# Kernel tuning notes

Hardware: AMD Instinct MI355X
Metric: run time of the kernel (lower is better)

The kernel has to match this reference:

```python
import jax, jax.numpy as jnp
import numpy as np

K = 3          # cfg.KNN_UP
CHUNK = 2048   # point chunk for brute-force KNN
BN_EPS = 1e-5


def knn_interp(vox_c, vox_f, pt_c):
    """Inverse-distance k-NN interpolation of voxel features onto points.
    vox_c: [Nv,3] voxel centers; vox_f: [Nv,C]; pt_c: [Np,3]. Returns [Np,C]."""
    Np = pt_c.shape[0]

    def chunk_fn(pc):  # pc: [CHUNK,3]
        d2 = jnp.sum((pc[:, None, :] - vox_c[None, :, :]) ** 2, axis=-1)  # [CHUNK,Nv]
        neg_d2, idx = jax.lax.top_k(-d2, K)                               # k nearest
        d = jnp.sqrt(jnp.maximum(-neg_d2, 0.0))
        w = 1.0 / (d + 1e-8)
        w = w / jnp.sum(w, axis=-1, keepdims=True)                        # [CHUNK,K]
        return jnp.sum(vox_f[idx] * w[..., None], axis=1)                 # [CHUNK,C]

    out = jax.lax.map(chunk_fn, pt_c.reshape(Np // CHUNK, CHUNK, 3))
    return out.reshape(Np, vox_f.shape[-1])


def bn1d(x, gamma, beta):
    # BatchNorm1d in training mode, applied per decomposed batch item (as in
    # the original per-sample list comprehension): stats over the point dim.
    mu = jnp.mean(x, axis=0, keepdims=True)
    var = jnp.var(x, axis=0, keepdims=True)
    return gamma * (x - mu) * jax.lax.rsqrt(var + BN_EPS) + beta


def level_forward(vox_c, vox_f, pt_c, gamma, beta):
    f = jax.vmap(knn_interp, in_axes=(0, 0, 0))(vox_c, vox_f, pt_c)  # [B,Np,C]
    return jax.vmap(lambda xf: bn1d(xf, gamma, beta))(f)


def setup_inputs() -> dict:
    key = jax.random.key(0)
    ks = jax.random.split(key, 16)
    B, Np = 2, 32768
    SCENE = 50.0  # spread coordinates over a ~50m scene
    nvs = [2048, 6144, 16384, 32768]
    chs = [256, 128, 96, 96]
    inp = {"pt_c": jax.random.uniform(ks[0], (B, Np, 3), jnp.float32) * SCENE}
    for i, (nv, c) in enumerate(zip(nvs, chs), start=1):
        inp[f"vox_c{i}"] = jax.random.uniform(ks[2 * i - 1], (B, nv, 3), jnp.float32) * SCENE
        inp[f"vox_f{i}"] = jax.random.normal(ks[2 * i], (B, nv, c), jnp.float32)
        inp[f"gamma{i}"] = jnp.ones((c,), jnp.float32)
        inp[f"beta{i}"] = jnp.zeros((c,), jnp.float32)
    return inp


def reference(pt_c, vox_c1, vox_f1, gamma1, beta1,
              vox_c2, vox_f2, gamma2, beta2,
              vox_c3, vox_f3, gamma3, beta3,
              vox_c4, vox_f4, gamma4, beta4):
    # voxel_to_point: per-level KNN upsampling of decoder voxel features to
    # the raw point cloud, followed by per-sample BatchNorm1d.
    f1 = level_forward(vox_c1, vox_f1, pt_c, gamma1, beta1)
    f2 = level_forward(vox_c2, vox_f2, pt_c, gamma2, beta2)
    f3 = level_forward(vox_c3, vox_f3, pt_c, gamma3, beta3)
    f4 = level_forward(vox_c4, vox_f4, pt_c, gamma4, beta4)
    return (f1, f2, f3, f4)
```

## Files before the change

kernel.cpp:

```cpp
#include <hip/hip_runtime.h>
#include <cfloat>
#include <climits>
#include <cstdint>

#define NPOINTS 32768
#define NBATCH  2
#define NLEV    4
#define NJOB    5
#define PG      16
#define PCELLS  (PG*PG*PG)
#define NPB     128
#define NBLK    (NPOINTS / NPB)

struct BinJob {
  const float* coords;
  int* cnt; int* start; int* cur;
  float4* sorted;
  int G, ncells, N;
  float invh;
};
struct BinParams { BinJob job[NJOB]; };

struct Level {
  const float4* sorted;
  const int*    start;
  int*          idxo;
  float*        wo;
  int G, ncells, Nv;
  float h, invh;
};
struct Params { Level lv[NLEV]; };

struct ApplyParams {
  const float* scale[NLEV];
  const float* shift[NLEV];
};

__device__ __forceinline__ int cell1d(float x, float invh, int G) {
  int c = (int)(x * invh);
  return min(max(c, 0), G - 1);
}

__global__ __launch_bounds__(256) void zero_kernel(int* __restrict__ p, int n)
{
  int i = blockIdx.x * 256 + threadIdx.x;
  if (i < n) p[i] = 0;
}

__global__ __launch_bounds__(256) void count_kernel(BinParams prm)
{
  const BinJob J = prm.job[blockIdx.z];
  int v = blockIdx.x * 256 + threadIdx.x;
  int b = blockIdx.y;
  if (v >= J.N) return;
  const float* p = J.coords + ((size_t)b * J.N + v) * 3;
  int cx = cell1d(p[0], J.invh, J.G), cy = cell1d(p[1], J.invh, J.G), cz = cell1d(p[2], J.invh, J.G);
  atomicAdd(&J.cnt[b * J.ncells + (cz * J.G + cy) * J.G + cx], 1);
}

__global__ __launch_bounds__(1024) void scan_kernel(BinParams prm)
{
  const BinJob J = prm.job[blockIdx.y];
  const int b = blockIdx.x, t = threadIdx.x;
  const int ncells = J.ncells;
  const int* c  = J.cnt + (size_t)b * ncells;
  int* st = J.start + (size_t)b * (ncells + 1);
  int* cu = J.cur + (size_t)b * ncells;
  __shared__ int part[1024];
  const int chunk = (ncells + 1023) / 1024;
  const int lo = t * chunk, hi = min(lo + chunk, ncells);
  int s = 0;
  for (int i = lo; i < hi; ++i) s += c[i];
  part[t] = s;
  __syncthreads();
  for (int off = 1; off < 1024; off <<= 1) {
    int v = (t >= off) ? part[t - off] : 0;
    __syncthreads();
    part[t] += v;
    __syncthreads();
  }
  int base = (t > 0) ? part[t - 1] : 0;
  for (int i = lo; i < hi; ++i) { st[i] = base; cu[i] = base; base += c[i]; }
  if (t == 1023) st[ncells] = part[1023];
}

__global__ __launch_bounds__(256) void scatter_kernel(BinParams prm)
{
  const BinJob J = prm.job[blockIdx.z];
  int v = blockIdx.x * 256 + threadIdx.x;
  int b = blockIdx.y;
  if (v >= J.N) return;
  const float* p = J.coords + ((size_t)b * J.N + v) * 3;
  float x = p[0], y = p[1], z = p[2];
  int cx = cell1d(x, J.invh, J.G), cy = cell1d(y, J.invh, J.G), cz = cell1d(z, J.invh, J.G);
  int pos = atomicAdd(&J.cur[b * J.ncells + (cz * J.G + cy) * J.G + cx], 1);
  J.sorted[(size_t)b * J.N + pos] = make_float4(x, y, z, __int_as_float(v));
}

__global__ __launch_bounds__(256) void phase1_kernel(
    const float4* __restrict__ psorted, Params prm,
    unsigned* __restrict__ taillist, int* __restrict__ tailcnt)
{
  const int l = blockIdx.y, b = blockIdx.z;
  const Level L = prm.lv[l];
  const int tid = threadIdx.x;
  const int q = tid & 3;
  const int sp = blockIdx.x * 64 + (tid >> 2);
  float4 pt = psorted[(size_t)b * NPOINTS + sp];
  const float px = pt.x, py = pt.y, pz = pt.z;
  const int p = __float_as_int(pt.w);
  const int G = L.G;
  const float h = L.h;

  const int cx = cell1d(px, L.invh, G);
  const int cy = cell1d(py, L.invh, G);
  const int cz = cell1d(pz, L.invh, G);
  const float fx = px - cx * h, fy = py - cy * h, fz = pz - cz * h;
  float m = fminf(fminf(fminf(fx, h - fx), fminf(fy, h - fy)), fminf(fz, h - fz));
  m = fmaxf(m, 0.f);

  const int* start     = L.start  + (size_t)b * (L.ncells + 1);
  const float4* sorted = L.sorted + (size_t)b * L.Nv;

  float b0 = FLT_MAX, b1 = FLT_MAX, b2 = FLT_MAX;
  int   i0 = INT_MAX, i1 = INT_MAX, i2 = INT_MAX;

  auto ins = [&](float d2, int vi) {
    if (d2 < b2 || (d2 == b2 && vi < i2)) {
      if (d2 < b1 || (d2 == b1 && vi < i1)) {
        b2 = b1; i2 = i1;
        if (d2 < b0 || (d2 == b0 && vi < i0)) { b1 = b0; i1 = i0; b0 = d2; i0 = vi; }
        else                                  { b1 = d2; i1 = vi; }
      } else { b2 = d2; i2 = vi; }
    }
  };
  auto cand = [&](int k) {
    float4 vv = sorted[k];
    int vi = __float_as_int(vv.w);
    float dx = px - vv.x, dy = py - vv.y, dz = pz - vv.z;
    float d2 = __fadd_rn(__fadd_rn(__fmul_rn(dx, dx), __fmul_rn(dy, dy)),
                         __fmul_rn(dz, dz));
    ins(d2, vi);
  };

  {
    const int x0 = max(cx - 1, 0), x1 = min(cx + 1, G - 1);
    int ks9[9], ke9[9];
    #pragma unroll
    for (int i = 0; i < 9; ++i) {
      const int dz = i / 3 - 1, dy = i % 3 - 1;
      const int iz = cz + dz, iy = cy + dy;
      const bool ok = (iz >= 0) && (iz < G) && (iy >= 0) && (iy < G);
      const int row = (iz * G + iy) * G;
      const int sa = ok ? (row + x0) : 0;
      const int sb = ok ? (row + x1 + 1) : 0;
      int a = start[sa], e = start[sb];
      if (!ok) { a = 0; e = 0; }
      ks9[i] = a; ke9[i] = e;
    }
    #pragma unroll
    for (int i = 0; i < 9; ++i)
      for (int k = ks9[i] + q; k < ke9[i]; k += 4) cand(k);
  }

  #pragma unroll
  for (int mask = 1; mask <= 2; mask <<= 1) {
    float c0 = __shfl_xor(b0, mask), c1 = __shfl_xor(b1, mask), c2 = __shfl_xor(b2, mask);
    int   j0 = __shfl_xor(i0, mask), j1 = __shfl_xor(i1, mask), j2 = __shfl_xor(i2, mask);
    ins(c0, j0); ins(c1, j1); ins(c2, j2);
  }

  float dmin = h + m;
  bool contained = (dmin * dmin * 0.99999f > b2);

  if (q == 0) {
    if (contained) {
      float w0 = 1.0f / (sqrtf(b0) + 1e-8f);
      float w1 = 1.0f / (sqrtf(b1) + 1e-8f);
      float w2 = 1.0f / (sqrtf(b2) + 1e-8f);
      float ws = (w0 + w1) + w2;
      size_t o = ((size_t)b * NPOINTS + p) * 3;
      L.idxo[o] = i0; L.idxo[o + 1] = i1; L.idxo[o + 2] = i2;
      L.wo[o] = w0 / ws; L.wo[o + 1] = w1 / ws; L.wo[o + 2] = w2 / ws;
    } else {
      int slot = atomicAdd(tailcnt, 1);
      taillist[slot] = (unsigned)sp | ((unsigned)l << 15) | ((unsigned)b << 17);
    }
  }
}

__global__ __launch_bounds__(256) void tail_kernel(
    const float4* __restrict__ psorted, Params prm,
    const unsigned* __restrict__ taillist, const int* __restrict__ tailcnt)
{
  const int tid = threadIdx.x;
  const int q = tid & 3;
  const int ent = blockIdx.x * 64 + (tid >> 2);
  const int n = *tailcnt;
  if (ent >= n) return;

  unsigned e = taillist[ent];
  const int sp = e & 0x7fff;
  const int l  = (e >> 15) & 3;
  const int b  = (e >> 17) & 1;
  const Level L = prm.lv[l];
  float4 pt = psorted[(size_t)b * NPOINTS + sp];
  const float px = pt.x, py = pt.y, pz = pt.z;
  const int p = __float_as_int(pt.w);
  const int G = L.G;
  const float h = L.h;

  const int cx = cell1d(px, L.invh, G);
  const int cy = cell1d(py, L.invh, G);
  const int cz = cell1d(pz, L.invh, G);
  const float fx = px - cx * h, fy = py - cy * h, fz = pz - cz * h;
  float m = fminf(fminf(fminf(fx, h - fx), fminf(fy, h - fy)), fminf(fz, h - fz));
  m = fmaxf(m, 0.f);

  const int* start     = L.start  + (size_t)b * (L.ncells + 1);
  const float4* sorted = L.sorted + (size_t)b * L.Nv;

  float b0 = FLT_MAX, b1 = FLT_MAX, b2 = FLT_MAX;
  int   i0 = INT_MAX, i1 = INT_MAX, i2 = INT_MAX;

  auto ins = [&](float d2, int vi) {
    if (d2 < b2 || (d2 == b2 && vi < i2)) {
      if (d2 < b1 || (d2 == b1 && vi < i1)) {
        b2 = b1; i2 = i1;
        if (d2 < b0 || (d2 == b0 && vi < i0)) { b1 = b0; i1 = i0; b0 = d2; i0 = vi; }
        else                                  { b1 = d2; i1 = vi; }
      } else { b2 = d2; i2 = vi; }
    }
  };
  auto cand = [&](int k) {
    float4 vv = sorted[k];
    int vi = __float_as_int(vv.w);
    float dx = px - vv.x, dy = py - vv.y, dz = pz - vv.z;
    float d2 = __fadd_rn(__fadd_rn(__fmul_rn(dx, dx), __fmul_rn(dy, dy)),
                         __fmul_rn(dz, dz));
    ins(d2, vi);
  };
  auto scan_range = [&](int ks, int ke) {
    for (int k = ks + q; k < ke; k += 4) cand(k);
  };

  const int rmax = max(max(cx, G - 1 - cx), max(max(cy, G - 1 - cy), max(cz, G - 1 - cz)));
  for (int rho = 0; rho <= rmax; ++rho) {
    if (rho >= 1) {
      float bm = fminf(b2, __shfl_xor(b2, 1));
      bm = fminf(bm, __shfl_xor(bm, 2));
      float dmin = fmaxf((rho - 1) * h + m, 0.f);
      if (dmin * dmin * 0.99999f > bm) break;
    }
    const int z0 = max(cz - rho, 0), z1 = min(cz + rho, G - 1);
    const int y0 = max(cy - rho, 0), y1 = min(cy + rho, G - 1);
    for (int iz = z0; iz <= z1; ++iz) {
      const int adz = abs(iz - cz);
      for (int iy = y0; iy <= y1; ++iy) {
        const int ady = max(adz, abs(iy - cy));
        const int row = (iz * G + iy) * G;
        if (ady == rho) {
          const int xa = max(cx - rho, 0), xb = min(cx + rho, G - 1);
          scan_range(start[row + xa], start[row + xb + 1]);
        } else {
          const int xl = cx - rho, xr = cx + rho;
          if (xl >= 0)     scan_range(start[row + xl], start[row + xl + 1]);
          if (xr <= G - 1) scan_range(start[row + xr], start[row + xr + 1]);
        }
      }
    }
  }

  #pragma unroll
  for (int mask = 1; mask <= 2; mask <<= 1) {
    float c0 = __shfl_xor(b0, mask), c1 = __shfl_xor(b1, mask), c2 = __shfl_xor(b2, mask);
    int   j0 = __shfl_xor(i0, mask), j1 = __shfl_xor(i1, mask), j2 = __shfl_xor(i2, mask);
    ins(c0, j0); ins(c1, j1); ins(c2, j2);
  }

  if (q == 0) {
    float w0 = 1.0f / (sqrtf(b0) + 1e-8f);
    float w1 = 1.0f / (sqrtf(b1) + 1e-8f);
    float w2 = 1.0f / (sqrtf(b2) + 1e-8f);
    float ws = (w0 + w1) + w2;
    size_t o = ((size_t)b * NPOINTS + p) * 3;
    L.idxo[o] = i0; L.idxo[o + 1] = i1; L.idxo[o + 2] = i2;
    L.wo[o] = w0 / ws; L.wo[o + 1] = w1 / ws; L.wo[o + 2] = w2 / ws;
  }
}

template <int C, int BDIM>
__global__ __launch_bounds__(BDIM) void interp_kernel(
    const float* __restrict__ voxf, const int* __restrict__ idxo,
    const float* __restrict__ wo, float* __restrict__ out,
    float* __restrict__ psum, float* __restrict__ psq, int Nv)
{
  constexpr int C4 = C / 4;
  constexpr int R  = BDIM / C4;
  const int b = blockIdx.y, blk = blockIdx.x;
  const int tid = threadIdx.x;
  const int r = tid / C4, c4 = tid - r * C4;
  const float4* fb = (const float4*)(voxf + (size_t)b * Nv * C);
  float4* ob = (float4*)(out + (size_t)b * NPOINTS * C);
  const int p0 = blk * NPB;

  float4 s = make_float4(0, 0, 0, 0), q = make_float4(0, 0, 0, 0);
  for (int p = p0 + r; p < p0 + NPB; p += R) {
    size_t pg = ((size_t)b * NPOINTS + p) * 3;
    int   ia = idxo[pg], ib = idxo[pg + 1], ic = idxo[pg + 2];
    float wa = wo[pg],   wb = wo[pg + 1],   wc = wo[pg + 2];
    float4 fa = fb[(size_t)ia * C4 + c4];
    float4 f2 = fb[(size_t)ib * C4 + c4];
    float4 fc = fb[(size_t)ic * C4 + c4];
    float4 o;
    o.x = wa * fa.x + wb * f2.x + wc * fc.x;
    o.y = wa * fa.y + wb * f2.y + wc * fc.y;
    o.z = wa * fa.z + wb * f2.z + wc * fc.z;
    o.w = wa * fa.w + wb * f2.w + wc * fc.w;
    ob[(size_t)p * C4 + c4] = o;
    s.x += o.x; s.y += o.y; s.z += o.z; s.w += o.w;
    q.x += o.x * o.x; q.y += o.y * o.y; q.z += o.z * o.z; q.w += o.w * o.w;
  }

  __shared__ float4 ls[BDIM];
  ls[tid] = s;
  __syncthreads();
  if (r == 0) {
    float4 tot = s;
    #pragma unroll
    for (int rr = 1; rr < R; ++rr) {
      float4 v = ls[c4 + rr * C4];
      tot.x += v.x; tot.y += v.y; tot.z += v.z; tot.w += v.w;
    }
    ((float4*)psum)[((size_t)b * NBLK + blk) * C4 + c4] = tot;
  }
  __syncthreads();
  ls[tid] = q;
  __syncthreads();
  if (r == 0) {
    float4 tot = q;
    #pragma unroll
    for (int rr = 1; rr < R; ++rr) {
      float4 v = ls[c4 + rr * C4];
      tot.x += v.x; tot.y += v.y; tot.z += v.z; tot.w += v.w;
    }
    ((float4*)psq)[((size_t)b * NBLK + blk) * C4 + c4] = tot;
  }
}

__global__ __launch_bounds__(256) void bn_stats_kernel(
    const float* __restrict__ psum, const float* __restrict__ psq,
    const float* __restrict__ gamma, const float* __restrict__ beta,
    float* __restrict__ scale, float* __restrict__ shift, int C, float invN)
{
  const int c = blockIdx.x, b = blockIdx.y, t = threadIdx.x;
  float s = 0.f, q = 0.f;
  for (int k = t; k < NBLK; k += 256) {
    s += psum[((size_t)b * NBLK + k) * C + c];
    q += psq[((size_t)b * NBLK + k) * C + c];
  }
  __shared__ float ss[256], qs[256];
  ss[t] = s; qs[t] = q;
  __syncthreads();
  for (int o = 128; o > 0; o >>= 1) {
    if (t < o) { ss[t] += ss[t + o]; qs[t] += qs[t + o]; }
    __syncthreads();
  }
  if (t == 0) {
    float mu  = ss[0] * invN;
    float var = fmaxf(qs[0] * invN - mu * mu, 0.f);
    float sc  = gamma[c] * rsqrtf(var + 1e-5f);
    scale[b * C + c] = sc;
    shift[b * C + c] = beta[c] - mu * sc;
  }
}

#define O1 4194304
#define O2 6291456
#define O3 7864320
__global__ __launch_bounds__(256) void bn_apply_all_kernel(
    float* __restrict__ out, ApplyParams ap)
{
  const int e = blockIdx.x * 256 + threadIdx.x;
  int l, base, C4;
  if (e < O1)      { l = 0; base = 0;  C4 = 64; }
  else if (e < O2) { l = 1; base = O1; C4 = 32; }
  else if (e < O3) { l = 2; base = O2; C4 = 24; }
  else             { l = 3; base = O3; C4 = 24; }
  const int local = e - base;
  const int npc4 = NPOINTS * C4;
  const int b = local / npc4;
  const int rem = local - b * npc4;
  const int c4 = rem % C4;
  float4 v  = ((float4*)out)[e];
  float4 sc = ((const float4*)ap.scale[l])[b * C4 + c4];
  float4 sh = ((const float4*)ap.shift[l])[b * C4 + c4];
  v.x = fmaf(v.x, sc.x, sh.x);
  v.y = fmaf(v.y, sc.y, sh.y);
  v.z = fmaf(v.z, sc.z, sh.z);
  v.w = fmaf(v.w, sc.w, sh.w);
  ((float4*)out)[e] = v;
}

extern "C" void kernel_launch(void* const* d_in, const int* in_sizes, int n_in,
                              void* d_out, int out_size, void* d_ws, size_t ws_size,
                              hipStream_t stream)
{
  const float* ptc = (const float*)d_in[0];
  static const int    Cs[4]     = {256, 128, 96, 96};
  static const int    Nvs[4]    = {2048, 6144, 16384, 32768};
  static const int    Gs[4]     = {10, 14, 18, 22};
  static const size_t outOff[4] = {0, 16777216, 25165824, 31457280};

  size_t off = 0;
  auto carve = [&](size_t bytes) {
    off = (off + 255) & ~(size_t)255;
    size_t o = off; off += bytes; return o;
  };
  char* w = (char*)d_ws;

  int nc[NJOB];
  for (int l = 0; l < 4; ++l) nc[l] = Gs[l] * Gs[l] * Gs[l];
  nc[4] = PCELLS;
  int Ns[NJOB] = {Nvs[0], Nvs[1], Nvs[2], Nvs[3], NPOINTS};
  int Gj[NJOB] = {Gs[0], Gs[1], Gs[2], Gs[3], PG};

  int totcnt = 0;
  for (int j = 0; j < NJOB; ++j) totcnt += nc[j];
  int* cntbase = (int*)(w + carve(((size_t)NBATCH * totcnt + 1) * 4));
  int* tailcnt = cntbase + (size_t)NBATCH * totcnt;

  float4* sortedj[NJOB]; int* cntj[NJOB]; int* sttj[NJOB]; int* curj[NJOB];
  {
    int acc = 0;
    for (int j = 0; j < NJOB; ++j) {
      cntj[j] = cntbase + (size_t)NBATCH * acc;
      acc += nc[j];
    }
  }
  for (int j = 0; j < NJOB; ++j) {
    sortedj[j] = (float4*)(w + carve((size_t)NBATCH * Ns[j] * 16));
    sttj[j]    = (int*)   (w + carve((size_t)NBATCH * (nc[j] + 1) * 4));
    curj[j]    = (int*)   (w + carve((size_t)NBATCH * nc[j] * 4));
  }
  int*      idxo   = (int*)     (w + carve((size_t)NLEV * NBATCH * NPOINTS * 3 * 4));
  float*    wo     = (float*)   (w + carve((size_t)NLEV * NBATCH * NPOINTS * 3 * 4));
  unsigned* taillist = (unsigned*)(w + carve((size_t)NLEV * NBATCH * NPOINTS * 4));
  float*    psum   = (float*)   (w + carve((size_t)NBATCH * NBLK * 256 * 4));
  float*    psq    = (float*)   (w + carve((size_t)NBATCH * NBLK * 256 * 4));
  float*    scale4[4]; float* shift4[4];
  for (int l = 0; l < 4; ++l) {
    scale4[l] = (float*)(w + carve((size_t)NBATCH * 256 * 4));
    shift4[l] = (float*)(w + carve((size_t)NBATCH * 256 * 4));
  }

  BinParams bp;
  for (int j = 0; j < NJOB; ++j) {
    BinJob& J = bp.job[j];
    J.coords = (j < 4) ? (const float*)d_in[1 + 4 * j] : ptc;
    J.cnt = cntj[j]; J.start = sttj[j]; J.cur = curj[j]; J.sorted = sortedj[j];
    J.G = Gj[j]; J.ncells = nc[j]; J.N = Ns[j];
    J.invh = Gj[j] / 50.0f;
  }

  Params prm;
  for (int l = 0; l < 4; ++l) {
    Level& L = prm.lv[l];
    L.sorted = sortedj[l]; L.start = sttj[l];
    L.idxo = idxo + (size_t)l * NBATCH * NPOINTS * 3;
    L.wo   = wo   + (size_t)l * NBATCH * NPOINTS * 3;
    L.G = Gs[l]; L.ncells = nc[l]; L.Nv = Nvs[l];
    L.h = 50.0f / Gs[l]; L.invh = Gs[l] / 50.0f;
  }

  ApplyParams ap;
  for (int l = 0; l < 4; ++l) { ap.scale[l] = scale4[l]; ap.shift[l] = shift4[l]; }

  const int zn = NBATCH * totcnt + 1;
  zero_kernel<<<(zn + 255) / 256, 256, 0, stream>>>(cntbase, zn);
  count_kernel<<<dim3((NPOINTS + 255) / 256, NBATCH, NJOB), 256, 0, stream>>>(bp);
  scan_kernel<<<dim3(NBATCH, NJOB), 1024, 0, stream>>>(bp);
  scatter_kernel<<<dim3((NPOINTS + 255) / 256, NBATCH, NJOB), 256, 0, stream>>>(bp);

  phase1_kernel<<<dim3(NPOINTS / 64, NLEV, NBATCH), 256, 0, stream>>>(
      sortedj[4], prm, taillist, tailcnt);
  tail_kernel<<<(NLEV * NBATCH * NPOINTS) / 64, 256, 0, stream>>>(
      sortedj[4], prm, taillist, tailcnt);

  for (int l = 0; l < 4; ++l) {
    const float* voxf  = (const float*)d_in[2 + 4 * l];
    const float* gamma = (const float*)d_in[3 + 4 * l];
    const float* beta  = (const float*)d_in[4 + 4 * l];
    const int C = Cs[l], Nv = Nvs[l];
    float* outl = (float*)d_out + outOff[l];
    const int* idl = idxo + (size_t)l * NBATCH * NPOINTS * 3;
    const float* wl = wo  + (size_t)l * NBATCH * NPOINTS * 3;

    if (C == 256)
      interp_kernel<256, 256><<<dim3(NBLK, NBATCH), 256, 0, stream>>>(
          voxf, idl, wl, outl, psum, psq, Nv);
    else if (C == 128)
      interp_kernel<128, 256><<<dim3(NBLK, NBATCH), 256, 0, stream>>>(
          voxf, idl, wl, outl, psum, psq, Nv);
    else
      interp_kernel<96, 240><<<dim3(NBLK, NBATCH), 240, 0, stream>>>(
          voxf, idl, wl, outl, psum, psq, Nv);

    bn_stats_kernel<<<dim3(C, NBATCH), 256, 0, stream>>>(
        psum, psq, gamma, beta, scale4[l], shift4[l], C, 1.0f / NPOINTS);
  }

  const int n4tot = 9437184;
  bn_apply_all_kernel<<<n4tot / 256, 256, 0, stream>>>((float*)d_out, ap);
}
```

Baseline: 391.9 us.

## Assign a full wavefront per tail point and distribute cell rows across lanes

The tail KNN kernel now gives each leftover point a whole 64-lane wavefront instead of 4 lanes. Cell rows of each search shell are dealt round-robin to lanes, and each lane scans its rows serially before a 64-wide shuffle merge. The kernel becomes a grid-stride loop over a fixed grid of 4096 blocks. This aims to cut the latency of hard points with large search radii, at the cost of more reduction shuffles and idle lanes when a shell has few rows.

```diff
diff --git a/kernel.cpp b/kernel.cpp
--- a/kernel.cpp
+++ b/kernel.cpp
@@ -193,99 +193,101 @@
     const float4* __restrict__ psorted, Params prm,
     const unsigned* __restrict__ taillist, const int* __restrict__ tailcnt)
 {
-  const int tid = threadIdx.x;
-  const int q = tid & 3;
-  const int ent = blockIdx.x * 64 + (tid >> 2);
+  const int lane = threadIdx.x & 63;
   const int n = *tailcnt;
-  if (ent >= n) return;
-
-  unsigned e = taillist[ent];
-  const int sp = e & 0x7fff;
-  const int l  = (e >> 15) & 3;
-  const int b  = (e >> 17) & 1;
-  const Level L = prm.lv[l];
-  float4 pt = psorted[(size_t)b * NPOINTS + sp];
-  const float px = pt.x, py = pt.y, pz = pt.z;
-  const int p = __float_as_int(pt.w);
-  const int G = L.G;
-  const float h = L.h;
-
-  const int cx = cell1d(px, L.invh, G);
-  const int cy = cell1d(py, L.invh, G);
-  const int cz = cell1d(pz, L.invh, G);
-  const float fx = px - cx * h, fy = py - cy * h, fz = pz - cz * h;
-  float m = fminf(fminf(fminf(fx, h - fx), fminf(fy, h - fy)), fminf(fz, h - fz));
-  m = fmaxf(m, 0.f);
-
-  const int* start     = L.start  + (size_t)b * (L.ncells + 1);
-  const float4* sorted = L.sorted + (size_t)b * L.Nv;
-
-  float b0 = FLT_MAX, b1 = FLT_MAX, b2 = FLT_MAX;
-  int   i0 = INT_MAX, i1 = INT_MAX, i2 = INT_MAX;
-
-  auto ins = [&](float d2, int vi) {
-    if (d2 < b2 || (d2 == b2 && vi < i2)) {
-      if (d2 < b1 || (d2 == b1 && vi < i1)) {
-        b2 = b1; i2 = i1;
-        if (d2 < b0 || (d2 == b0 && vi < i0)) { b1 = b0; i1 = i0; b0 = d2; i0 = vi; }
-        else                                  { b1 = d2; i1 = vi; }
-      } else { b2 = d2; i2 = vi; }
-    }
-  };
-  auto cand = [&](int k) {
-    float4 vv = sorted[k];
-    int vi = __float_as_int(vv.w);
-    float dx = px - vv.x, dy = py - vv.y, dz = pz - vv.z;
-    float d2 = __fadd_rn(__fadd_rn(__fmul_rn(dx, dx), __fmul_rn(dy, dy)),
-                         __fmul_rn(dz, dz));
-    ins(d2, vi);
-  };
-  auto scan_range = [&](int ks, int ke) {
-    for (int k = ks + q; k < ke; k += 4) cand(k);
-  };
-
-  const int rmax = max(max(cx, G - 1 - cx), max(max(cy, G - 1 - cy), max(cz, G - 1 - cz)));
-  for (int rho = 0; rho <= rmax; ++rho) {
-    if (rho >= 1) {
-      float bm = fminf(b2, __shfl_xor(b2, 1));
-      bm = fminf(bm, __shfl_xor(bm, 2));
-      float dmin = fmaxf((rho - 1) * h + m, 0.f);
-      if (dmin * dmin * 0.99999f > bm) break;
-    }
-    const int z0 = max(cz - rho, 0), z1 = min(cz + rho, G - 1);
-    const int y0 = max(cy - rho, 0), y1 = min(cy + rho, G - 1);
-    for (int iz = z0; iz <= z1; ++iz) {
-      const int adz = abs(iz - cz);
-      for (int iy = y0; iy <= y1; ++iy) {
-        const int ady = max(adz, abs(iy - cy));
-        const int row = (iz * G + iy) * G;
-        if (ady == rho) {
-          const int xa = max(cx - rho, 0), xb = min(cx + rho, G - 1);
-          scan_range(start[row + xa], start[row + xb + 1]);
-        } else {
-          const int xl = cx - rho, xr = cx + rho;
-          if (xl >= 0)     scan_range(start[row + xl], start[row + xl + 1]);
-          if (xr <= G - 1) scan_range(start[row + xr], start[row + xr + 1]);
+
+  for (int ent = blockIdx.x * 4 + (threadIdx.x >> 6); ent < n; ent += gridDim.x * 4) {
+    unsigned e = taillist[ent];
+    const int sp = e & 0x7fff;
+    const int l  = (e >> 15) & 3;
+    const int b  = (e >> 17) & 1;
+    const Level L = prm.lv[l];
+    float4 pt = psorted[(size_t)b * NPOINTS + sp];
+    const float px = pt.x, py = pt.y, pz = pt.z;
+    const int p = __float_as_int(pt.w);
+    const int G = L.G;
+    const float h = L.h;
+
+    const int cx = cell1d(px, L.invh, G);
+    const int cy = cell1d(py, L.invh, G);
+    const int cz = cell1d(pz, L.invh, G);
+    const float fx = px - cx * h, fy = py - cy * h, fz = pz - cz * h;
+    float m = fminf(fminf(fminf(fx, h - fx), fminf(fy, h - fy)), fminf(fz, h - fz));
+    m = fmaxf(m, 0.f);
+
+    const int* start     = L.start  + (size_t)b * (L.ncells + 1);
+    const float4* sorted = L.sorted + (size_t)b * L.Nv;
+
+    float b0 = FLT_MAX, b1 = FLT_MAX, b2 = FLT_MAX;
+    int   i0 = INT_MAX, i1 = INT_MAX, i2 = INT_MAX;
+
+    auto ins = [&](float d2, int vi) {
+      if (d2 < b2 || (d2 == b2 && vi < i2)) {
+        if (d2 < b1 || (d2 == b1 && vi < i1)) {
+          b2 = b1; i2 = i1;
+          if (d2 < b0 || (d2 == b0 && vi < i0)) { b1 = b0; i1 = i0; b0 = d2; i0 = vi; }
+          else                                  { b1 = d2; i1 = vi; }
+        } else { b2 = d2; i2 = vi; }
+      }
+    };
+    auto scan_row = [&](int ks, int ke) {
+      for (int k = ks; k < ke; ++k) {
+        float4 vv = sorted[k];
+        int vi = __float_as_int(vv.w);
+        float dx = px - vv.x, dy = py - vv.y, dz = pz - vv.z;
+        float d2 = __fadd_rn(__fadd_rn(__fmul_rn(dx, dx), __fmul_rn(dy, dy)),
+                             __fmul_rn(dz, dz));
+        ins(d2, vi);
+      }
+    };
+
+    const int rmax = max(max(cx, G - 1 - cx), max(max(cy, G - 1 - cy), max(cz, G - 1 - cz)));
+    for (int rho = 0; rho <= rmax; ++rho) {
+      if (rho >= 1) {
+        float bm = b2;
+        #pragma unroll
+        for (int mask = 1; mask < 64; mask <<= 1) bm = fminf(bm, __shfl_xor(bm, mask));
+        float dmn = fmaxf((rho - 1) * h + m, 0.f);
+        if (dmn * dmn * 0.99999f > bm) break;
+      }
+      const int z0 = max(cz - rho, 0), z1 = min(cz + rho, G - 1);
+      const int y0 = max(cy - rho, 0), y1 = min(cy + rho, G - 1);
+      int task = 0;
+      for (int iz = z0; iz <= z1; ++iz) {
+        const int adz = abs(iz - cz);
+        for (int iy = y0; iy <= y1; ++iy) {
+          const int ady = max(adz, abs(iy - cy));
+          const int row = (iz * G + iy) * G;
+          if (ady == rho) {
+            if ((task++ & 63) == lane) {
+              const int xa = max(cx - rho, 0), xb = min(cx + rho, G - 1);
+              scan_row(start[row + xa], start[row + xb + 1]);
+            }
+          } else {
+            const int xl = cx - rho, xr = cx + rho;
+            if (xl >= 0)     { if ((task++ & 63) == lane) scan_row(start[row + xl], start[row + xl + 1]); }
+            if (xr <= G - 1) { if ((task++ & 63) == lane) scan_row(start[row + xr], start[row + xr + 1]); }
+          }
         }
       }
     }
-  }
-
-  #pragma unroll
-  for (int mask = 1; mask <= 2; mask <<= 1) {
-    float c0 = __shfl_xor(b0, mask), c1 = __shfl_xor(b1, mask), c2 = __shfl_xor(b2, mask);
-    int   j0 = __shfl_xor(i0, mask), j1 = __shfl_xor(i1, mask), j2 = __shfl_xor(i2, mask);
-    ins(c0, j0); ins(c1, j1); ins(c2, j2);
-  }
-
-  if (q == 0) {
-    float w0 = 1.0f / (sqrtf(b0) + 1e-8f);
-    float w1 = 1.0f / (sqrtf(b1) + 1e-8f);
-    float w2 = 1.0f / (sqrtf(b2) + 1e-8f);
-    float ws = (w0 + w1) + w2;
-    size_t o = ((size_t)b * NPOINTS + p) * 3;
-    L.idxo[o] = i0; L.idxo[o + 1] = i1; L.idxo[o + 2] = i2;
-    L.wo[o] = w0 / ws; L.wo[o + 1] = w1 / ws; L.wo[o + 2] = w2 / ws;
+
+    #pragma unroll
+    for (int mask = 1; mask <= 32; mask <<= 1) {
+      float c0 = __shfl_xor(b0, mask), c1 = __shfl_xor(b1, mask), c2 = __shfl_xor(b2, mask);
+      int   j0 = __shfl_xor(i0, mask), j1 = __shfl_xor(i1, mask), j2 = __shfl_xor(i2, mask);
+      ins(c0, j0); ins(c1, j1); ins(c2, j2);
+    }
+
+    if (lane == 0) {
+      float w0 = 1.0f / (sqrtf(b0) + 1e-8f);
+      float w1 = 1.0f / (sqrtf(b1) + 1e-8f);
+      float w2 = 1.0f / (sqrtf(b2) + 1e-8f);
+      float ws = (w0 + w1) + w2;
+      size_t o = ((size_t)b * NPOINTS + p) * 3;
+      L.idxo[o] = i0; L.idxo[o + 1] = i1; L.idxo[o + 2] = i2;
+      L.wo[o] = w0 / ws; L.wo[o + 1] = w1 / ws; L.wo[o + 2] = w2 / ws;
+    }
   }
 }
 
@@ -484,8 +486,7 @@
 
   phase1_kernel<<<dim3(NPOINTS / 64, NLEV, NBATCH), 256, 0, stream>>>(
       sortedj[4], prm, taillist, tailcnt);
-  tail_kernel<<<(NLEV * NBATCH * NPOINTS) / 64, 256, 0, stream>>>(
-      sortedj[4], prm, taillist, tailcnt);
+  tail_kernel<<<4096, 256, 0, stream>>>(sortedj[4], prm, taillist, tailcnt);
 
   for (int l = 0; l < 4; ++l) {
     const float* voxf  = (const float*)d_in[2 + 4 * l];
```

After: 444.2 us. 13.3% more time.
